# Kernel optimization log

Hardware: AMD Instinct MI355X
Metric: run time of the kernel (lower is better)

## Reference

```python
import jax, jax.numpy as jnp
import numpy as np

B, C, H, W = 1, 320, 64, 64
HEADS, DHEAD = 8, 40
INNER = HEADS * DHEAD          # 320 == C (as in Stable Diffusion)
CTX_LEN, CTX_DIM = 77, 768
FF_INNER = 4 * INNER           # 1280
GROUPS, GN_EPS, LN_EPS = 32, 1e-6, 1e-5
SCALE = DHEAD ** -0.5


def setup_inputs() -> dict:
    key = jax.random.key(0)
    ks = jax.random.split(key, 16)
    def w(k, shape):
        return jax.random.normal(k, shape, jnp.float32) * 0.02
    return {
        'x': jax.random.normal(ks[0], (B, C, H, W), jnp.float32),
        'context': jax.random.normal(ks[1], (B, CTX_LEN, CTX_DIM), jnp.float32),
        'gn_scale': jnp.ones((C,), jnp.float32),
        'gn_bias': jnp.zeros((C,), jnp.float32),
        'w_proj_in': w(ks[2], (C, INNER)), 'b_proj_in': jnp.zeros((INNER,), jnp.float32),
        'ln1_s': jnp.ones((INNER,), jnp.float32), 'ln1_b': jnp.zeros((INNER,), jnp.float32),
        'wq1': w(ks[3], (INNER, INNER)), 'wk1': w(ks[4], (INNER, INNER)),
        'wv1': w(ks[5], (INNER, INNER)), 'wo1': w(ks[6], (INNER, INNER)),
        'bo1': jnp.zeros((INNER,), jnp.float32),
        'ln2_s': jnp.ones((INNER,), jnp.float32), 'ln2_b': jnp.zeros((INNER,), jnp.float32),
        'wq2': w(ks[7], (INNER, INNER)), 'wk2': w(ks[8], (CTX_DIM, INNER)),
        'wv2': w(ks[9], (CTX_DIM, INNER)), 'wo2': w(ks[10], (INNER, INNER)),
        'bo2': jnp.zeros((INNER,), jnp.float32),
        'ln3_s': jnp.ones((INNER,), jnp.float32), 'ln3_b': jnp.zeros((INNER,), jnp.float32),
        'w_ff1': w(ks[11], (INNER, 2 * FF_INNER)), 'b_ff1': jnp.zeros((2 * FF_INNER,), jnp.float32),
        'w_ff2': w(ks[12], (FF_INNER, INNER)), 'b_ff2': jnp.zeros((INNER,), jnp.float32),
        'w_proj_out': w(ks[13], (INNER, C)), 'b_proj_out': jnp.zeros((C,), jnp.float32),
    }


def _group_norm(x, scale, bias):
    b, c, h, w = x.shape
    xg = x.reshape(b, GROUPS, c // GROUPS, h, w)
    mu = xg.mean(axis=(2, 3, 4), keepdims=True)
    var = xg.var(axis=(2, 3, 4), keepdims=True)
    xg = (xg - mu) * jax.lax.rsqrt(var + GN_EPS)
    return xg.reshape(b, c, h, w) * scale[None, :, None, None] + bias[None, :, None, None]


def _layer_norm(x, s, b):
    mu = x.mean(-1, keepdims=True)
    var = x.var(-1, keepdims=True)
    return (x - mu) * jax.lax.rsqrt(var + LN_EPS) * s + b


def _attention(xq, ctx, wq, wk, wv, wo, bo):
    b, s, _ = xq.shape
    t = ctx.shape[1]
    q = (xq @ wq).reshape(b, s, HEADS, DHEAD)
    k = (ctx @ wk).reshape(b, t, HEADS, DHEAD)
    v = (ctx @ wv).reshape(b, t, HEADS, DHEAD)
    scores = jnp.einsum('bihd,bjhd->bhij', q, k) * SCALE  # [b,h,s,t]
    probs = jax.nn.softmax(scores, axis=-1)
    o = jnp.einsum('bhij,bjhd->bihd', probs, v).reshape(b, s, INNER)
    return o @ wo + bo


def _forward(x, context, gn_scale, gn_bias, w_proj_in, b_proj_in,
             ln1_s, ln1_b, wq1, wk1, wv1, wo1, bo1,
             ln2_s, ln2_b, wq2, wk2, wv2, wo2, bo2,
             ln3_s, ln3_b, w_ff1, b_ff1, w_ff2, b_ff2,
             w_proj_out, b_proj_out):
    x_in = x
    h_ = _group_norm(x, gn_scale, gn_bias)
    # 1x1 conv proj_in as channel matmul
    h_ = jnp.einsum('bchw,cd->bdhw', h_, w_proj_in) + b_proj_in[None, :, None, None]
    h_ = h_.transpose(0, 2, 3, 1).reshape(B, H * W, INNER)  # [b, s, d]
    # self-attention
    hn = _layer_norm(h_, ln1_s, ln1_b)
    h_ = _attention(hn, hn, wq1, wk1, wv1, wo1, bo1) + h_
    # cross-attention
    hn = _layer_norm(h_, ln2_s, ln2_b)
    h_ = _attention(hn, context, wq2, wk2, wv2, wo2, bo2) + h_
    # GEGLU feed-forward
    hn = _layer_norm(h_, ln3_s, ln3_b)
    y = hn @ w_ff1 + b_ff1
    a, g = jnp.split(y, 2, axis=-1)
    y = (a * jax.nn.gelu(g, approximate=False)) @ w_ff2 + b_ff2
    h_ = y + h_
    h_ = h_.reshape(B, H, W, INNER).transpose(0, 3, 1, 2)
    out = jnp.einsum('bchw,cd->bdhw', h_, w_proj_out) + b_proj_out[None, :, None, None]
    return out + x_in


def reference(x, context, gn_scale, gn_bias, w_proj_in, b_proj_in,
              ln1_s, ln1_b, wq1, wk1, wv1, wo1, bo1,
              ln2_s, ln2_b, wq2, wk2, wv2, wo2, bo2,
              ln3_s, ln3_b, w_ff1, b_ff1, w_ff2, b_ff2,
              w_proj_out, b_proj_out):
    return _forward(x, context, gn_scale, gn_bias, w_proj_in, b_proj_in,
                    ln1_s, ln1_b, wq1, wk1, wv1, wo1, bo1,
                    ln2_s, ln2_b, wq2, wk2, wv2, wo2, bo2,
                    ln3_s, ln3_b, w_ff1, b_ff1, w_ff2, b_ff2,
                    w_proj_out, b_proj_out)
```

## Files before the change

### kernel.cpp

```cpp
#include <hip/hip_runtime.h>
#include <hip/hip_bf16.h>
#include <math.h>

#define SCALE_L2E  0.22811011265722836f

typedef __attribute__((ext_vector_type(8))) short short8v;
typedef __attribute__((ext_vector_type(4))) float float4v;
typedef unsigned short u16;

__device__ __forceinline__ unsigned pack2(float a, float b) {
  float2 f; f.x = a; f.y = b;
  __hip_bfloat162 h = __float22bfloat162_rn(f);
  return *(unsigned*)&h;
}
__device__ __forceinline__ float bfu2f(u16 u) {
  return __uint_as_float(((unsigned)u) << 16);
}
__device__ __forceinline__ u16 f2bf(float x) {
  __hip_bfloat16 h = __float2bfloat16(x);
  return *(u16*)&h;
}

struct TDesc { const float* src; u16* dst; int K, N, off, tx; float sc; };
struct TPack { TDesc d[12]; };

__global__ __launch_bounds__(256) void prep_kernel(
    TPack p, int nT,
    const float* __restrict__ ctxsrc, u16* __restrict__ ctxdst,
    const float* __restrict__ x,
    float* __restrict__ psum, float* __restrict__ psq) {
  __shared__ float ls[32][33];
  int bt = blockIdx.x, t = threadIdx.x;
  if (bt < nT) {
    int ti = 0;
    #pragma unroll
    for (int i = 1; i < 12; i++) if (bt >= p.d[i].off) ti = i;
    TDesc dd = p.d[ti];
    int local = bt - dd.off;
    int n0 = (local % dd.tx) * 32, k0 = (local / dd.tx) * 32;
    #pragma unroll
    for (int i = 0; i < 4; i++) {
      int idx = t + i*256, r = idx >> 5, c = idx & 31;
      ls[r][c] = dd.src[(size_t)(k0 + r)*dd.N + n0 + c];
    }
    __syncthreads();
    #pragma unroll
    for (int i = 0; i < 2; i++) {
      int p2 = t + i*256, n = p2 >> 4, kp = (p2 & 15)*2;
      *(unsigned*)&dd.dst[(size_t)(n0 + n)*dd.K + k0 + kp] =
        pack2(ls[kp][n]*dd.sc, ls[kp+1][n]*dd.sc);
    }
  } else if (bt < nT + 58) {
    int idx = ((bt - nT)*256 + t)*4;
    if (idx < 59136) {
      float4 v = *(const float4*)&ctxsrc[idx];
      uint2 o; o.x = pack2(v.x, v.y); o.y = pack2(v.z, v.w);
      *(uint2*)&ctxdst[idx] = o;
    }
  } else {
    int pp = bt - nT - 58;
    int g = pp >> 3, part = pp & 7;
    size_t base = (size_t)g*40960 + (size_t)part*5120;
    float sum = 0.f, sq = 0.f;
    #pragma unroll
    for (int r = 0; r < 5; r++) {
      float4 v = *(const float4*)&x[base + (size_t)(t + r*256)*4];
      sum += v.x + v.y + v.z + v.w;
      sq  += v.x*v.x + v.y*v.y + v.z*v.z + v.w*v.w;
    }
    float* s1 = &ls[0][0];
    float* s2 = &ls[8][0] + 8;
    s1[t] = sum; s2[t] = sq; __syncthreads();
    for (int st = 128; st > 0; st >>= 1) {
      if (t < st) { s1[t] += s1[t+st]; s2[t] += s2[t+st]; }
      __syncthreads();
    }
    if (t == 0) { psum[pp] = s1[0]; psq[pp] = s2[0]; }
  }
}

__global__ __launch_bounds__(256) void gn_kcvc(
    const float* __restrict__ x, const float* __restrict__ psum,
    const float* __restrict__ psq, const float* __restrict__ gs,
    const float* __restrict__ gb, u16* __restrict__ gnT,
    const u16* __restrict__ ctxb, const u16* __restrict__ wk2T,
    u16* __restrict__ kcvc) {
  __shared__ __align__(16) u16 smem[2*64*72];
  __shared__ float scl[64], sft[64];
  const int t = threadIdx.x;
  if (blockIdx.x < 320) {
    float* ts = (float*)smem;
    int s0 = (blockIdx.x & 63) * 64, c0 = (blockIdx.x >> 6) * 64;
    if (t < 64) {
      int c = c0 + t, g = c / 10;
      float s = 0.f, q = 0.f;
      #pragma unroll
      for (int i = 0; i < 8; i++) { s += psum[g*8 + i]; q += psq[g*8 + i]; }
      float mu = s * (1.f/40960.f);
      float var = q * (1.f/40960.f) - mu*mu;
      float rs = rsqrtf(var + 1e-6f);
      float sc = rs * gs[c];
      scl[t] = sc;
      sft[t] = gb[c] - mu * sc;
    }
    int crow = t >> 2, sch = (t & 3) * 16;
    #pragma unroll
    for (int j = 0; j < 4; j++) {
      float4 v = *(const float4*)&x[(size_t)(c0 + crow)*4096 + s0 + sch + 4*j];
      ts[crow*65 + sch + 4*j + 0] = v.x; ts[crow*65 + sch + 4*j + 1] = v.y;
      ts[crow*65 + sch + 4*j + 2] = v.z; ts[crow*65 + sch + 4*j + 3] = v.w;
    }
    __syncthreads();
    int srow = t >> 2, cch = (t & 3) * 16;
    #pragma unroll
    for (int p = 0; p < 8; p++) {
      int cl = cch + 2*p;
      float f0 = ts[cl*65 + srow] * scl[cl] + sft[cl];
      float f1 = ts[(cl+1)*65 + srow] * scl[cl+1] + sft[cl+1];
      *(unsigned*)&gnT[(size_t)(s0 + srow)*320 + c0 + cl] = pack2(f0, f1);
    }
  } else {
    u16* As = smem;
    u16* Bs = smem + 64*72;
    const int lane = t & 63, w = t >> 6, l16 = lane & 15, g = lane >> 4;
    int local = blockIdx.x - 320;
    const int bm = (local & 1) * 64, bn = (local >> 1) * 64;
    const int m0 = (w & 1) * 32, n0 = (w >> 1) * 32;
    float4v acc[2][2] = {};
    const int ar = t >> 2, ac = (t & 3) * 16;
    const bool aok = (bm + ar) < 77;
    const u16* ga = &ctxb[(size_t)(bm + ar)*768 + ac];
    const u16* gbp = &wk2T[(size_t)(bn + ar)*768 + ac];
    short8v pa0 = {}, pa1 = {}, pb0, pb1;
    if (aok) { pa0 = *(const short8v*)ga; pa1 = *(const short8v*)(ga + 8); }
    pb0 = *(const short8v*)gbp; pb1 = *(const short8v*)(gbp + 8);
    for (int k0 = 0; k0 < 768; k0 += 64) {
      __syncthreads();
      *(short8v*)&As[ar*72 + ac] = pa0;
      *(short8v*)&As[ar*72 + ac + 8] = pa1;
      *(short8v*)&Bs[ar*72 + ac] = pb0;
      *(short8v*)&Bs[ar*72 + ac + 8] = pb1;
      __syncthreads();
      if (k0 + 64 < 768) {
        if (aok) { pa0 = *(const short8v*)(ga + k0 + 64); pa1 = *(const short8v*)(ga + k0 + 72); }
        pb0 = *(const short8v*)(gbp + k0 + 64); pb1 = *(const short8v*)(gbp + k0 + 72);
      }
      #pragma unroll
      for (int ks = 0; ks < 2; ks++) {
        short8v af[2], bfv[2];
        #pragma unroll
        for (int mt = 0; mt < 2; mt++)
          af[mt] = *(const short8v*)&As[(m0 + 16*mt + l16)*72 + ks*32 + g*8];
        #pragma unroll
        for (int nt = 0; nt < 2; nt++)
          bfv[nt] = *(const short8v*)&Bs[(n0 + 16*nt + l16)*72 + ks*32 + g*8];
        #pragma unroll
        for (int mt = 0; mt < 2; mt++)
          #pragma unroll
          for (int nt = 0; nt < 2; nt++)
            acc[mt][nt] = __builtin_amdgcn_mfma_f32_16x16x32_bf16(af[mt], bfv[nt], acc[mt][nt], 0, 0, 0);
      }
    }
    __syncthreads();
    float* Cs = (float*)smem;
    #pragma unroll
    for (int mt = 0; mt < 2; mt++)
      #pragma unroll
      for (int nt = 0; nt < 2; nt++)
        #pragma unroll
        for (int r = 0; r < 4; r++)
          Cs[(m0 + 16*mt + 4*g + r)*68 + n0 + 16*nt + l16] = acc[mt][nt][r];
    __syncthreads();
    u16* C = kcvc + (size_t)(bn / 320) * 24640;
    int nb = bn % 320;
    #pragma unroll
    for (int i = 0; i < 8; i++) {
      int p = t + i*256;
      int mm = p >> 5, nn = (p & 31)*2;
      if (bm + mm >= 77) continue;
      *(unsigned*)&C[(size_t)(bm + mm)*320 + nb + nn] = pack2(Cs[mm*68 + nn], Cs[mm*68 + nn + 1]);
    }
  }
}

__global__ __launch_bounds__(64) void layernorm_kernel(
    const u16* __restrict__ X, const float* __restrict__ s,
    const float* __restrict__ b, u16* __restrict__ Y) {
  int row = blockIdx.x, t = threadIdx.x;
  const u16* xr = X + (size_t)row*320;
  float v[5], sum = 0.f, sq = 0.f;
  #pragma unroll
  for (int i = 0; i < 5; i++) { v[i] = bfu2f(xr[t + 64*i]); sum += v[i]; sq += v[i]*v[i]; }
  #pragma unroll
  for (int o = 32; o > 0; o >>= 1) { sum += __shfl_down(sum, o); sq += __shfl_down(sq, o); }
  sum = __shfl(sum, 0); sq = __shfl(sq, 0);
  float mu = sum * (1.f/320.f);
  float var = sq * (1.f/320.f) - mu*mu;
  float rs = rsqrtf(var + 1e-5f);
  u16* yr = Y + (size_t)row*320;
  #pragma unroll
  for (int i = 0; i < 5; i++) {
    int c = t + 64*i;
    yr[c] = f2bf((v[i]-mu)*rs*s[c] + b[c]);
  }
}

template<int MODE>
__global__ __launch_bounds__(256) void oneshot(
    const u16* __restrict__ A, const u16* __restrict__ BT,
    const float* __restrict__ bias, const u16* __restrict__ res,
    const float* __restrict__ xres, void* __restrict__ Cout,
    int K, int chunks) {
  __shared__ __align__(16) u16 As[64*328];
  __shared__ __align__(16) u16 Bs[32*328];
  const int t = threadIdx.x;
  const int lane = t & 63, w = t >> 6, l16 = lane & 15, g = lane >> 4;
  const int bm = blockIdx.x * 64, bn = blockIdx.y * 32;
  const int m0 = (w & 1) * 32, n0 = (w >> 1) * 16;
  float4v acc[2] = {};

  const u16* Ab = A + (size_t)(bm + (t>>2))*K + (t&3)*16;
  u16* Al = As + (t>>2)*328 + (t&3)*16;
  const u16* Bb = BT + (size_t)(bn + (t>>3))*K + (t&7)*16;
  u16* Bl = Bs + (t>>3)*328 + (t&7)*16;
  const bool b3 = (t & 7) < 4;

  for (int ch = 0; ch < chunks; ch++) {
    const int c0 = ch*320;
    __syncthreads();
    #pragma unroll
    for (int j = 0; j < 5; j++) {
      *(short8v*)(Al + 64*j)     = *(const short8v*)(Ab + c0 + 64*j);
      *(short8v*)(Al + 64*j + 8) = *(const short8v*)(Ab + c0 + 64*j + 8);
    }
    *(short8v*)Bl         = *(const short8v*)(Bb + c0);
    *(short8v*)(Bl + 8)   = *(const short8v*)(Bb + c0 + 8);
    *(short8v*)(Bl + 128) = *(const short8v*)(Bb + c0 + 128);
    *(short8v*)(Bl + 136) = *(const short8v*)(Bb + c0 + 136);
    if (b3) {
      *(short8v*)(Bl + 256) = *(const short8v*)(Bb + c0 + 256);
      *(short8v*)(Bl + 264) = *(const short8v*)(Bb + c0 + 264);
    }
    __syncthreads();
    #pragma unroll
    for (int ks = 0; ks < 10; ks++) {
      short8v bfv = *(const short8v*)&Bs[(n0 + l16)*328 + ks*32 + g*8];
      #pragma unroll
      for (int mt = 0; mt < 2; mt++) {
        short8v af = *(const short8v*)&As[(m0 + 16*mt + l16)*328 + ks*32 + g*8];
        acc[mt] = __builtin_amdgcn_mfma_f32_16x16x32_bf16(af, bfv, acc[mt], 0, 0, 0);
      }
    }
  }
  __syncthreads();
  float* Cs = (float*)As;
  #pragma unroll
  for (int mt = 0; mt < 2; mt++)
    #pragma unroll
    for (int r = 0; r < 4; r++)
      Cs[(m0 + 16*mt + 4*g + r)*36 + n0 + l16] = acc[mt][r];
  __syncthreads();

  if (MODE == 0) {
    u16* C = (u16*)Cout;
    #pragma unroll
    for (int i = 0; i < 4; i++) {
      int p = t + i*256;
      int mm = p >> 4, pp = (p & 15)*2;
      float f0 = Cs[mm*36 + pp], f1 = Cs[mm*36 + pp + 1];
      if (bias) { f0 += bias[bn + pp]; f1 += bias[bn + pp + 1]; }
      if (res) {
        unsigned u = *(const unsigned*)&res[(size_t)(bm + mm)*320 + bn + pp];
        f0 += bfu2f((u16)(u & 0xffffu));
        f1 += bfu2f((u16)(u >> 16));
      }
      *(unsigned*)&C[(size_t)(bm + mm)*320 + bn + pp] = pack2(f0, f1);
    }
  } else {
    float* C = (float*)Cout;
    int nloc = t >> 3, mch = (t & 7) * 8;
    float bb = bias[bn + nloc];
    #pragma unroll
    for (int j = 0; j < 2; j++) {
      int m4 = mch + j*4;
      float4 xv = *(const float4*)&xres[(size_t)(bn + nloc)*4096 + bm + m4];
      float4 ov;
      ov.x = Cs[(m4+0)*36 + nloc] + bb + xv.x;
      ov.y = Cs[(m4+1)*36 + nloc] + bb + xv.y;
      ov.z = Cs[(m4+2)*36 + nloc] + bb + xv.z;
      ov.w = Cs[(m4+3)*36 + nloc] + bb + xv.w;
      *(float4*)&C[(size_t)(bn + nloc)*4096 + bm + m4] = ov;
    }
  }
}

__global__ __launch_bounds__(256) void qkv_oneshot(
    const u16* __restrict__ A, const u16* __restrict__ BT,
    u16* __restrict__ qk, u16* __restrict__ vT, int segStride) {
  __shared__ __align__(16) u16 As[64*328];
  __shared__ __align__(16) u16 Bs[32*328];
  const int t = threadIdx.x;
  const int lane = t & 63, w = t >> 6, l16 = lane & 15, g = lane >> 4;
  const int bm = blockIdx.x * 64, bn = blockIdx.y * 32;
  const int m0 = (w & 1) * 32, n0 = (w >> 1) * 16;
  float4v acc[2] = {};

  const u16* Ab = A + (size_t)(bm + (t>>2))*320 + (t&3)*16;
  u16* Al = As + (t>>2)*328 + (t&3)*16;
  const u16* Bb = BT + (size_t)(bn + (t>>3))*320 + (t&7)*16;
  u16* Bl = Bs + (t>>3)*328 + (t&7)*16;
  const bool b3 = (t & 7) < 4;

  #pragma unroll
  for (int j = 0; j < 5; j++) {
    *(short8v*)(Al + 64*j)     = *(const short8v*)(Ab + 64*j);
    *(short8v*)(Al + 64*j + 8) = *(const short8v*)(Ab + 64*j + 8);
  }
  *(short8v*)Bl         = *(const short8v*)Bb;
  *(short8v*)(Bl + 8)   = *(const short8v*)(Bb + 8);
  *(short8v*)(Bl + 128) = *(const short8v*)(Bb + 128);
  *(short8v*)(Bl + 136) = *(const short8v*)(Bb + 136);
  if (b3) {
    *(short8v*)(Bl + 256) = *(const short8v*)(Bb + 256);
    *(short8v*)(Bl + 264) = *(const short8v*)(Bb + 264);
  }
  __syncthreads();
  #pragma unroll
  for (int ks = 0; ks < 10; ks++) {
    short8v bfv = *(const short8v*)&Bs[(n0 + l16)*328 + ks*32 + g*8];
    #pragma unroll
    for (int mt = 0; mt < 2; mt++) {
      short8v af = *(const short8v*)&As[(m0 + 16*mt + l16)*328 + ks*32 + g*8];
      acc[mt] = __builtin_amdgcn_mfma_f32_16x16x32_bf16(af, bfv, acc[mt], 0, 0, 0);
    }
  }
  __syncthreads();
  float* Cs = (float*)As;
  #pragma unroll
  for (int mt = 0; mt < 2; mt++)
    #pragma unroll
    for (int r = 0; r < 4; r++)
      Cs[(m0 + 16*mt + 4*g + r)*36 + n0 + l16] = acc[mt][r];
  __syncthreads();

  if (bn < 640) {
    u16* C = qk + (size_t)(bn / 320) * segStride;
    int nb = bn % 320;
    #pragma unroll
    for (int i = 0; i < 4; i++) {
      int p = t + i*256;
      int mm = p >> 4, pp = (p & 15)*2;
      *(unsigned*)&C[(size_t)(bm + mm)*320 + nb + pp] = pack2(Cs[mm*36 + pp], Cs[mm*36 + pp + 1]);
    }
  } else {
    int nloc = t >> 3, mch = (t & 7) * 8;
    int vd = bn - 640 + nloc;
    u16* dst = vT + (size_t)vd*4096 + bm + mch;
    uint4 o0;
    o0.x = pack2(Cs[(mch+0)*36 + nloc], Cs[(mch+1)*36 + nloc]);
    o0.y = pack2(Cs[(mch+2)*36 + nloc], Cs[(mch+3)*36 + nloc]);
    o0.z = pack2(Cs[(mch+4)*36 + nloc], Cs[(mch+5)*36 + nloc]);
    o0.w = pack2(Cs[(mch+6)*36 + nloc], Cs[(mch+7)*36 + nloc]);
    *(uint4*)dst = o0;
  }
}

__global__ __launch_bounds__(256) void geglu_mfma(
    const u16* __restrict__ A, const u16* __restrict__ BT,
    const float* __restrict__ bias, u16* __restrict__ C) {
  __shared__ __align__(16) u16 smem[3*64*72];
  u16* As = smem;
  u16* Ba = smem + 64*72;
  u16* Bg = smem + 2*64*72;
  const int t = threadIdx.x;
  const int lane = t & 63, w = t >> 6, l16 = lane & 15, g = lane >> 4;
  const int bm = blockIdx.x * 64, bn = blockIdx.y * 64;
  const int m0 = (w & 1) * 32, n0 = (w >> 1) * 32;
  float4v aacc[2][2] = {}, gacc[2][2] = {};
  const int ar = t >> 2, ac = (t & 3) * 16;
  const u16* ga  = &A[(size_t)(bm + ar)*320 + ac];
  const u16* gba = &BT[(size_t)(bn + ar)*320 + ac];
  const u16* gbg = &BT[(size_t)(1280 + bn + ar)*320 + ac];

  short8v pa0 = *(const short8v*)ga,  pa1 = *(const short8v*)(ga + 8);
  short8v pb0 = *(const short8v*)gba, pb1 = *(const short8v*)(gba + 8);
  short8v pg0 = *(const short8v*)gbg, pg1 = *(const short8v*)(gbg + 8);

  for (int k0 = 0; k0 < 320; k0 += 64) {
    __syncthreads();
    *(short8v*)&As[ar*72 + ac] = pa0;
    *(short8v*)&As[ar*72 + ac + 8] = pa1;
    *(short8v*)&Ba[ar*72 + ac] = pb0;
    *(short8v*)&Ba[ar*72 + ac + 8] = pb1;
    *(short8v*)&Bg[ar*72 + ac] = pg0;
    *(short8v*)&Bg[ar*72 + ac + 8] = pg1;
    __syncthreads();
    if (k0 + 64 < 320) {
      pa0 = *(const short8v*)(ga + k0 + 64);  pa1 = *(const short8v*)(ga + k0 + 72);
      pb0 = *(const short8v*)(gba + k0 + 64); pb1 = *(const short8v*)(gba + k0 + 72);
      pg0 = *(const short8v*)(gbg + k0 + 64); pg1 = *(const short8v*)(gbg + k0 + 72);
    }
    #pragma unroll
    for (int ks = 0; ks < 2; ks++) {
      short8v af[2], bav[2], bgv[2];
      #pragma unroll
      for (int mt = 0; mt < 2; mt++)
        af[mt] = *(const short8v*)&As[(m0 + 16*mt + l16)*72 + ks*32 + g*8];
      #pragma unroll
      for (int nt = 0; nt < 2; nt++) {
        bav[nt] = *(const short8v*)&Ba[(n0 + 16*nt + l16)*72 + ks*32 + g*8];
        bgv[nt] = *(const short8v*)&Bg[(n0 + 16*nt + l16)*72 + ks*32 + g*8];
      }
      #pragma unroll
      for (int mt = 0; mt < 2; mt++)
        #pragma unroll
        for (int nt = 0; nt < 2; nt++) {
          aacc[mt][nt] = __builtin_amdgcn_mfma_f32_16x16x32_bf16(af[mt], bav[nt], aacc[mt][nt], 0, 0, 0);
          gacc[mt][nt] = __builtin_amdgcn_mfma_f32_16x16x32_bf16(af[mt], bgv[nt], gacc[mt][nt], 0, 0, 0);
        }
    }
  }
  __syncthreads();
  float* Cs = (float*)smem;
  #pragma unroll
  for (int nt = 0; nt < 2; nt++) {
    int col = n0 + 16*nt + l16;
    float ba = bias[bn + col];
    float bg2 = bias[1280 + bn + col];
    #pragma unroll
    for (int mt = 0; mt < 2; mt++)
      #pragma unroll
      for (int r = 0; r < 4; r++) {
        float a = aacc[mt][nt][r] + ba;
        float gv = gacc[mt][nt][r] + bg2;
        float gl = 0.5f * gv * (1.f + erff(gv * 0.70710678118654752f));
        Cs[(m0 + 16*mt + 4*g + r)*68 + col] = a * gl;
      }
  }
  __syncthreads();
  #pragma unroll
  for (int i = 0; i < 8; i++) {
    int p = t + i*256;
    int mm = p >> 5, nn = (p & 31)*2;
    *(unsigned*)&C[(size_t)(bm + mm)*1280 + bn + nn] = pack2(Cs[mm*68 + nn], Cs[mm*68 + nn + 1]);
  }
}

__global__ __launch_bounds__(512) void self_attn_part(
    const u16* __restrict__ Q, const u16* __restrict__ K,
    const u16* __restrict__ vT, u16* __restrict__ Opart,
    float* __restrict__ Lp) {
  const int h = blockIdx.y;
  const int q0 = blockIdx.x * 128;
  const int sp = blockIdx.z;
  const int tid = threadIdx.x;
  const int w = tid >> 6, lane = tid & 63;
  const int l16 = lane & 15, g = lane >> 4;

  __shared__ __align__(16) u16 Kls[64][72];
  __shared__ __align__(16) u16 Vt[48][72];
  __shared__ __align__(16) u16 PsT[8][16][72];

  for (int e = tid; e < 64*12; e += 512) {
    int r = e / 12, c = e % 12;
    *(unsigned*)&Kls[r][40 + 2*c] = 0u;
  }
  if (tid < 256) {
    int r = 40 + (tid >> 5), c = tid & 31;
    *(unsigned*)&Vt[r][2*c] = (r == 40) ? 0x3F803F80u : 0u;
  }

  short8v Qb[2];
  {
    const u16* qrow = Q + (size_t)(q0 + w*16 + l16)*320 + h*40;
    Qb[0] = *(const short8v*)(qrow + g*8);
    short8v z = {};
    Qb[1] = (g == 0) ? *(const short8v*)(qrow + 32) : z;
  }

  const u16* Kbase = K + (size_t)(sp*1024)*320 + h*40;
  const u16* Vbase = vT + (size_t)(h*40)*4096 + sp*1024;

  const int ksl = (tid < 320) ? tid : 0;
  const int keyK = ksl / 5, chK = ksl - keyK*5;
  const u16* gK = Kbase + (size_t)keyK*320 + chK*8;
  u16* lK = &Kls[keyK][chK*8];
  const int vsl = (tid >= 192) ? (tid - 192) : 0;
  const int dV = vsl >> 3, chV = vsl & 7;
  const u16* gV = Vbase + (size_t)dV*4096 + chV*8;
  u16* lV = &Vt[dV][chV*8];

  const bool doK = (tid < 320), doV = (tid >= 192);

  short8v rK = {}, rV = {};
  if (doK) rK = *(const short8v*)gK;
  if (doV) rV = *(const short8v*)gV;
  gK += 64*320; gV += 64;

  float4v Of[3] = {};

  for (int it = 0; it < 16; ++it) {
    __syncthreads();
    if (doK) *(short8v*)lK = rK;
    if (doV) *(short8v*)lV = rV;
    __syncthreads();
    if (it < 15) {
      if (doK) rK = *(const short8v*)gK;
      if (doV) rV = *(const short8v*)gV;
      gK += 64*320; gV += 64;
    }

    float4v Sf[4];
    #pragma unroll
    for (int mt = 0; mt < 4; mt++) {
      short8v ka0 = *(const short8v*)&Kls[mt*16 + l16][g*8];
      short8v ka1 = *(const short8v*)&Kls[mt*16 + l16][32 + g*8];
      float4v s = {};
      s = __builtin_amdgcn_mfma_f32_16x16x32_bf16(ka0, Qb[0], s, 0, 0, 0);
      s = __builtin_amdgcn_mfma_f32_16x16x32_bf16(ka1, Qb[1], s, 0, 0, 0);
      Sf[mt] = s;
    }

    #pragma unroll
    for (int mt = 0; mt < 4; mt++)
      #pragma unroll
      for (int r = 0; r < 4; r++)
        Sf[mt][r] = exp2f(Sf[mt][r]);

    #pragma unroll
    for (int mt = 0; mt < 4; mt++) {
      uint2 pk;
      pk.x = pack2(Sf[mt][0], Sf[mt][1]);
      pk.y = pack2(Sf[mt][2], Sf[mt][3]);
      *(uint2*)&PsT[w][l16][mt*16 + 4*g] = pk;
    }
    asm volatile("s_waitcnt lgkmcnt(0)" ::: "memory");

    #pragma unroll
    for (int ks = 0; ks < 2; ks++) {
      short8v pb = *(const short8v*)&PsT[w][l16][ks*32 + g*8];
      #pragma unroll
      for (int mt = 0; mt < 3; mt++) {
        short8v va = *(const short8v*)&Vt[mt*16 + l16][ks*32 + g*8];
        Of[mt] = __builtin_amdgcn_mfma_f32_16x16x32_bf16(va, pb, Of[mt], 0, 0, 0);
      }
    }
  }

  const int q = q0 + w*16 + l16;
  u16* orow = Opart + (size_t)sp*4096*320 + (size_t)q*320 + h*40;
  #pragma unroll
  for (int mt = 0; mt < 3; mt++) {
    #pragma unroll
    for (int rp = 0; rp < 2; rp++) {
      int d = mt*16 + 4*g + rp*2;
      if (d < 40)
        *(unsigned*)&orow[d] = pack2(Of[mt][rp*2], Of[mt][rp*2+1]);
    }
  }
  if (g == 2)
    Lp[sp*32768 + q*8 + h] = Of[2][0];
}

__global__ __launch_bounds__(256) void attn_merge(
    const u16* __restrict__ Opart, const float* __restrict__ Lp,
    u16* __restrict__ O) {
  int gid = blockIdx.x*256 + threadIdx.x;
  int dp = gid % 20;
  int qh = gid / 20;
  int q = qh >> 3, h = qh & 7;
  float ls = Lp[qh] + Lp[32768 + qh] + Lp[2*32768 + qh] + Lp[3*32768 + qh];
  size_t base = (size_t)q*320 + h*40 + dp*2;
  const size_t HBu = 4096u*320u;
  float r0 = 0.f, r1 = 0.f;
  #pragma unroll
  for (int sp = 0; sp < 4; sp++) {
    unsigned u = *(const unsigned*)&Opart[sp*HBu + base];
    r0 += bfu2f((u16)(u & 0xffffu));
    r1 += bfu2f((u16)(u >> 16));
  }
  float inv = 1.f / ls;
  *(unsigned*)&O[base] = pack2(r0*inv, r1*inv);
}

__global__ __launch_bounds__(256) void cross_attn_mfma(
    const u16* __restrict__ Q, const u16* __restrict__ Kc,
    const u16* __restrict__ Vc, u16* __restrict__ O) {
  const int h = blockIdx.y;
  const int q0 = blockIdx.x * 64;
  const int tid = threadIdx.x;
  const int w = tid >> 6, lane = tid & 63;
  const int l16 = lane & 15, g = lane >> 4;

  __shared__ __align__(16) u16 Kls[80][72];
  __shared__ __align__(16) u16 Vt[48][104];
  __shared__ __align__(16) u16 PsT[4][16][104];

  for (int e = tid; e < 80*12; e += 256) {
    int r = e / 12, c = e % 12;
    *(unsigned*)&Kls[r][40 + 2*c] = 0u;
  }
  for (int e = tid; e < 48*52; e += 256) {
    int r = e / 52, c = e % 52;
    *(unsigned*)&Vt[r][2*c] = 0u;
  }
  {
    int r = lane >> 2, c4 = (lane & 3)*4;
    uint2 z; z.x = 0u; z.y = 0u;
    *(uint2*)&PsT[w][r][80 + c4] = z;
  }

  short8v Qb[2];
  {
    const u16* qrow = Q + (size_t)(q0 + w*16 + l16)*320 + h*40;
    Qb[0] = *(const short8v*)(qrow + g*8);
    short8v z = {};
    Qb[1] = (g == 0) ? *(const short8v*)(qrow + 32) : z;
  }

  for (int e = tid; e < 1600; e += 256) {
    int key = e / 20, dp = e % 20;
    unsigned val = 0u;
    if (key < 77) val = *(const unsigned*)&Kc[(size_t)key*320 + h*40 + dp*2];
    *(unsigned*)&Kls[key][dp*2] = val;
  }
  __syncthreads();
  for (int e = tid; e < 1600; e += 256) {
    int kp = e / 40, d = e % 40;
    unsigned u0 = (kp*2     < 77) ? (unsigned)Vc[(size_t)(kp*2    )*320 + h*40 + d] : 0u;
    unsigned u1 = (kp*2 + 1 < 77) ? (unsigned)Vc[(size_t)(kp*2 + 1)*320 + h*40 + d] : 0u;
    *(unsigned*)&Vt[d][kp*2] = u0 | (u1 << 16);
  }
  __syncthreads();

  float4v Sf[5];
  #pragma unroll
  for (int mt = 0; mt < 5; mt++) {
    short8v ka0 = *(const short8v*)&Kls[mt*16 + l16][g*8];
    short8v ka1 = *(const short8v*)&Kls[mt*16 + l16][32 + g*8];
    float4v s = {};
    s = __builtin_amdgcn_mfma_f32_16x16x32_bf16(ka0, Qb[0], s, 0, 0, 0);
    s = __builtin_amdgcn_mfma_f32_16x16x32_bf16(ka1, Qb[1], s, 0, 0, 0);
    Sf[mt] = s;
  }

  float rsum = 0.f;
  #pragma unroll
  for (int mt = 0; mt < 5; mt++)
    #pragma unroll
    for (int r = 0; r < 4; r++) {
      int key = mt*16 + 4*g + r;
      float p = (key < 77) ? exp2f(Sf[mt][r]) : 0.f;
      Sf[mt][r] = p; rsum += p;
    }
  rsum += __shfl_xor(rsum, 16);
  rsum += __shfl_xor(rsum, 32);

  #pragma unroll
  for (int mt = 0; mt < 5; mt++) {
    uint2 pk;
    pk.x = pack2(Sf[mt][0], Sf[mt][1]);
    pk.y = pack2(Sf[mt][2], Sf[mt][3]);
    *(uint2*)&PsT[w][l16][mt*16 + 4*g] = pk;
  }
  __syncthreads();

  float4v Of[3] = {};
  #pragma unroll
  for (int ks = 0; ks < 3; ks++) {
    short8v pb = *(const short8v*)&PsT[w][l16][ks*32 + g*8];
    #pragma unroll
    for (int mt = 0; mt < 3; mt++) {
      short8v va = *(const short8v*)&Vt[mt*16 + l16][ks*32 + g*8];
      Of[mt] = __builtin_amdgcn_mfma_f32_16x16x32_bf16(va, pb, Of[mt], 0, 0, 0);
    }
  }

  float inv = 1.f / rsum;
  u16* orow = O + (size_t)(q0 + w*16 + l16)*320 + h*40;
  #pragma unroll
  for (int mt = 0; mt < 3; mt++) {
    #pragma unroll
    for (int rp = 0; rp < 2; rp++) {
      int d = mt*16 + 4*g + rp*2;
      if (d < 40)
        *(unsigned*)&orow[d] = pack2(Of[mt][rp*2] * inv, Of[mt][rp*2+1] * inv);
    }
  }
}

extern "C" void kernel_launch(void* const* d_in, const int* in_sizes, int n_in,
                              void* d_out, int out_size, void* d_ws, size_t ws_size,
                              hipStream_t stream) {
  const float* x        = (const float*)d_in[0];
  const float* ctx      = (const float*)d_in[1];
  const float* gn_s     = (const float*)d_in[2];
  const float* gn_b     = (const float*)d_in[3];
  const float* w_pin    = (const float*)d_in[4];
  const float* b_pin    = (const float*)d_in[5];
  const float* ln1_s    = (const float*)d_in[6];
  const float* ln1_b    = (const float*)d_in[7];
  const float* wq1      = (const float*)d_in[8];
  const float* wk1      = (const float*)d_in[9];
  const float* wv1      = (const float*)d_in[10];
  const float* wo1      = (const float*)d_in[11];
  const float* bo1      = (const float*)d_in[12];
  const float* ln2_s    = (const float*)d_in[13];
  const float* ln2_b    = (const float*)d_in[14];
  const float* wq2      = (const float*)d_in[15];
  const float* wk2      = (const float*)d_in[16];
  const float* wv2      = (const float*)d_in[17];
  const float* wo2      = (const float*)d_in[18];
  const float* bo2      = (const float*)d_in[19];
  const float* ln3_s    = (const float*)d_in[20];
  const float* ln3_b    = (const float*)d_in[21];
  const float* w_ff1    = (const float*)d_in[22];
  const float* b_ff1    = (const float*)d_in[23];
  const float* w_ff2    = (const float*)d_in[24];
  const float* b_ff2    = (const float*)d_in[25];
  const float* w_pout   = (const float*)d_in[26];
  const float* b_pout   = (const float*)d_in[27];
  float* out = (float*)d_out;

  u16* ws = (u16*)d_ws;
  const size_t HB = 4096u*320u;
  u16* h   = ws;
  u16* hn  = ws + HB;
  u16* q   = ws + 2*HB;
  u16* k   = ws + 3*HB;
  u16* vT  = ws + 4*HB;
  u16* ao  = ws + 5*HB;
  u16* gnT = k;
  u16* gg  = q;
  u16* wb  = ws + 6*HB;
  size_t o = 0;
  u16* ctxb   = wb + o; o += 59136;
  u16* wq1T   = wb + o; o += 102400;
  u16* wk1T   = wb + o; o += 102400;
  u16* wv1T   = wb + o; o += 102400;
  u16* wo1T   = wb + o; o += 102400;
  u16* wq2T   = wb + o; o += 102400;
  u16* wk2T   = wb + o; o += 245760;
  u16* wv2T   = wb + o; o += 245760;
  u16* wo2T   = wb + o; o += 102400;
  u16* wff1T  = wb + o; o += 819200;
  u16* wff2T  = wb + o; o += 409600;
  u16* wpoutT = wb + o; o += 102400;
  u16* wpinT  = wb + o; o += 102400;
  u16* kc     = wb + o; o += 24640;
  u16* vc     = wb + o; o += 24640;
  float* psum = (float*)(wb + o);
  float* psq  = psum + 256;
  u16* OpartB = (u16*)(psq + 256);
  float* Lpart = (float*)(OpartB + 4*HB);

  TPack tp;
  const float* srcs[12] = {wq1, wk1, wv1, wo1, wq2, wo2, w_pin, w_pout, wk2, wv2, w_ff1, w_ff2};
  u16* dsts[12]         = {wq1T, wk1T, wv1T, wo1T, wq2T, wo2T, wpinT, wpoutT, wk2T, wv2T, wff1T, wff2T};
  int Ks[12] = {320,320,320,320,320,320,320,320,768,768,320,1280};
  int Ns[12] = {320,320,320,320,320,320,320,320,320,320,2560,320};
  int off = 0;
  for (int i = 0; i < 12; i++) {
    tp.d[i].src = srcs[i]; tp.d[i].dst = dsts[i];
    tp.d[i].K = Ks[i]; tp.d[i].N = Ns[i];
    tp.d[i].off = off; tp.d[i].tx = Ns[i]/32;
    tp.d[i].sc = (i == 0 || i == 4) ? SCALE_L2E : 1.0f;
    off += (Ks[i]/32)*(Ns[i]/32);
  }

  dim3 blk(256), g64x10(64, 10);
  const u16* nres = nullptr;
  const float* nb = nullptr;

  hipLaunchKernelGGL(prep_kernel, dim3(off + 58 + 256), blk, 0, stream,
                     tp, off, ctx, ctxb, x, psum, psq);
  hipLaunchKernelGGL(gn_kcvc, dim3(340), blk, 0, stream,
                     x, psum, psq, gn_s, gn_b, gnT, ctxb, wk2T, kc);
  hipLaunchKernelGGL((oneshot<0>), g64x10, blk, 0, stream, gnT, wpinT, b_pin, nres, nb, (void*)h, 320, 1);
  hipLaunchKernelGGL(layernorm_kernel, dim3(4096), dim3(64), 0, stream, h, ln1_s, ln1_b, hn);
  hipLaunchKernelGGL(qkv_oneshot, dim3(64, 30), blk, 0, stream, hn, wq1T, q, vT, (int)HB);
  hipLaunchKernelGGL(self_attn_part, dim3(32, 8, 4), dim3(512), 0, stream, q, k, vT, OpartB, Lpart);
  hipLaunchKernelGGL(attn_merge, dim3(2560), blk, 0, stream, OpartB, Lpart, ao);
  hipLaunchKernelGGL((oneshot<0>), g64x10, blk, 0, stream, ao, wo1T, bo1, h, nb, (void*)h, 320, 1);
  hipLaunchKernelGGL(layernorm_kernel, dim3(4096), dim3(64), 0, stream, h, ln2_s, ln2_b, hn);
  hipLaunchKernelGGL((oneshot<0>), g64x10, blk, 0, stream, hn, wq2T, nb, nres, nb, (void*)q, 320, 1);
  hipLaunchKernelGGL(cross_attn_mfma, dim3(64, 8), blk, 0, stream, q, kc, vc, ao);
  hipLaunchKernelGGL((oneshot<0>), g64x10, blk, 0, stream, ao, wo2T, bo2, h, nb, (void*)h, 320, 1);
  hipLaunchKernelGGL(layernorm_kernel, dim3(4096), dim3(64), 0, stream, h, ln3_s, ln3_b, hn);
  hipLaunchKernelGGL(geglu_mfma, dim3(64, 20), blk, 0, stream, hn, wff1T, b_ff1, gg);
  hipLaunchKernelGGL((oneshot<0>), g64x10, blk, 0, stream, gg, wff2T, b_ff2, h, nb, (void*)h, 1280, 4);
  hipLaunchKernelGGL((oneshot<2>), g64x10, blk, 0, stream, h, wpoutT, b_pout, nres, x, (void*)out, 320, 1);
}
```

Measured before the change: 289.7 us.

## Fuse LayerNorm into consuming GEMMs by folding affine params into weights

Removes the three standalone LayerNorm kernels and their bf16 round-trip through the hn buffer. The LN gain is folded into the transposed weight columns during prep, and the LN bias is folded into a per-output bias vector (W^T·b) computed by extra prep blocks. The consuming GEMMs (qkv, q2, geglu) now normalise each loaded row in registers before staging it to LDS. This trades extra per-block normalisation work (each output-column tile recomputes the row statistics) and a slightly different rounding order for fewer launches and less global memory traffic.

Measured after the change: 298.5 us. 3.0% more time.

```diff
diff --git a/kernel.cpp b/kernel.cpp
--- a/kernel.cpp
+++ b/kernel.cpp
@@ -16,16 +16,44 @@
 __device__ __forceinline__ float bfu2f(u16 u) {
   return __uint_as_float(((unsigned)u) << 16);
 }
-__device__ __forceinline__ u16 f2bf(float x) {
-  __hip_bfloat16 h = __float2bfloat16(x);
-  return *(u16*)&h;
-}
-
-struct TDesc { const float* src; u16* dst; int K, N, off, tx; float sc; };
+
+__device__ __forceinline__ void row_ln(short8v av[10]) {
+  float sum = 0.f, sq = 0.f;
+  #pragma unroll
+  for (int v = 0; v < 10; v++) {
+    union { short8v s; u16 u[8]; } t; t.s = av[v];
+    #pragma unroll
+    for (int e = 0; e < 8; e++) {
+      float f = bfu2f(t.u[e]);
+      sum += f; sq = fmaf(f, f, sq);
+    }
+  }
+  sum += __shfl_xor(sum, 1); sum += __shfl_xor(sum, 2);
+  sq  += __shfl_xor(sq, 1);  sq  += __shfl_xor(sq, 2);
+  float mu = sum * (1.f/320.f);
+  float var = sq * (1.f/320.f) - mu*mu;
+  float rs = rsqrtf(var + 1e-5f);
+  float cc = -mu * rs;
+  #pragma unroll
+  for (int v = 0; v < 10; v++) {
+    union { short8v s; u16 u[8]; unsigned w[4]; } t; t.s = av[v];
+    #pragma unroll
+    for (int e = 0; e < 4; e++) {
+      float f0 = fmaf(bfu2f(t.u[2*e]),   rs, cc);
+      float f1 = fmaf(bfu2f(t.u[2*e+1]), rs, cc);
+      t.w[e] = pack2(f0, f1);
+    }
+    av[v] = t.s;
+  }
+}
+
+struct TDesc { const float* src; u16* dst; const float* sv; int K, N, off, tx; float sc; };
 struct TPack { TDesc d[12]; };
+struct GDesc { const float* W; const float* bvec; const float* add; float* out; int K, N, off; float sc; };
+struct GPack { GDesc d[5]; };
 
 __global__ __launch_bounds__(256) void prep_kernel(
-    TPack p, int nT,
+    TPack p, GPack gp, int nT,
     const float* __restrict__ ctxsrc, u16* __restrict__ ctxdst,
     const float* __restrict__ x,
     float* __restrict__ psum, float* __restrict__ psq) {
@@ -47,8 +75,10 @@
     #pragma unroll
     for (int i = 0; i < 2; i++) {
       int p2 = t + i*256, n = p2 >> 4, kp = (p2 & 15)*2;
+      float s0 = dd.sc, s1 = dd.sc;
+      if (dd.sv) { s0 *= dd.sv[k0 + kp]; s1 *= dd.sv[k0 + kp + 1]; }
       *(unsigned*)&dd.dst[(size_t)(n0 + n)*dd.K + k0 + kp] =
-        pack2(ls[kp][n]*dd.sc, ls[kp+1][n]*dd.sc);
+        pack2(ls[kp][n]*s0, ls[kp+1][n]*s1);
     }
   } else if (bt < nT + 58) {
     int idx = ((bt - nT)*256 + t)*4;
@@ -57,7 +87,7 @@
       uint2 o; o.x = pack2(v.x, v.y); o.y = pack2(v.z, v.w);
       *(uint2*)&ctxdst[idx] = o;
     }
-  } else {
+  } else if (bt < nT + 58 + 256) {
     int pp = bt - nT - 58;
     int g = pp >> 3, part = pp & 7;
     size_t base = (size_t)g*40960 + (size_t)part*5120;
@@ -76,6 +106,22 @@
       __syncthreads();
     }
     if (t == 0) { psum[pp] = s1[0]; psq[pp] = s2[0]; }
+  } else {
+    int bg = bt - nT - 58 - 256;
+    int gi = 0;
+    #pragma unroll
+    for (int i = 1; i < 5; i++) if (bg >= gp.d[i].off) gi = i;
+    GDesc dd = gp.d[gi];
+    int n = (bg - dd.off)*256 + t;
+    if (n < dd.N) {
+      float acc = 0.f;
+      #pragma unroll 8
+      for (int k = 0; k < dd.K; k++)
+        acc = fmaf(dd.W[(size_t)k*dd.N + n], dd.bvec[k], acc);
+      acc *= dd.sc;
+      if (dd.add) acc += dd.add[n];
+      dd.out[n] = acc;
+    }
   }
 }
 
@@ -183,29 +229,7 @@
   }
 }
 
-__global__ __launch_bounds__(64) void layernorm_kernel(
-    const u16* __restrict__ X, const float* __restrict__ s,
-    const float* __restrict__ b, u16* __restrict__ Y) {
-  int row = blockIdx.x, t = threadIdx.x;
-  const u16* xr = X + (size_t)row*320;
-  float v[5], sum = 0.f, sq = 0.f;
-  #pragma unroll
-  for (int i = 0; i < 5; i++) { v[i] = bfu2f(xr[t + 64*i]); sum += v[i]; sq += v[i]*v[i]; }
-  #pragma unroll
-  for (int o = 32; o > 0; o >>= 1) { sum += __shfl_down(sum, o); sq += __shfl_down(sq, o); }
-  sum = __shfl(sum, 0); sq = __shfl(sq, 0);
-  float mu = sum * (1.f/320.f);
-  float var = sq * (1.f/320.f) - mu*mu;
-  float rs = rsqrtf(var + 1e-5f);
-  u16* yr = Y + (size_t)row*320;
-  #pragma unroll
-  for (int i = 0; i < 5; i++) {
-    int c = t + 64*i;
-    yr[c] = f2bf((v[i]-mu)*rs*s[c] + b[c]);
-  }
-}
-
-template<int MODE>
+template<int MODE, int LN>
 __global__ __launch_bounds__(256) void oneshot(
     const u16* __restrict__ A, const u16* __restrict__ BT,
     const float* __restrict__ bias, const u16* __restrict__ res,
@@ -228,10 +252,25 @@
   for (int ch = 0; ch < chunks; ch++) {
     const int c0 = ch*320;
     __syncthreads();
-    #pragma unroll
-    for (int j = 0; j < 5; j++) {
-      *(short8v*)(Al + 64*j)     = *(const short8v*)(Ab + c0 + 64*j);
-      *(short8v*)(Al + 64*j + 8) = *(const short8v*)(Ab + c0 + 64*j + 8);
+    if (LN) {
+      short8v av[10];
+      #pragma unroll
+      for (int j = 0; j < 5; j++) {
+        av[2*j]   = *(const short8v*)(Ab + 64*j);
+        av[2*j+1] = *(const short8v*)(Ab + 64*j + 8);
+      }
+      row_ln(av);
+      #pragma unroll
+      for (int j = 0; j < 5; j++) {
+        *(short8v*)(Al + 64*j)     = av[2*j];
+        *(short8v*)(Al + 64*j + 8) = av[2*j+1];
+      }
+    } else {
+      #pragma unroll
+      for (int j = 0; j < 5; j++) {
+        *(short8v*)(Al + 64*j)     = *(const short8v*)(Ab + c0 + 64*j);
+        *(short8v*)(Al + 64*j + 8) = *(const short8v*)(Ab + c0 + 64*j + 8);
+      }
     }
     *(short8v*)Bl         = *(const short8v*)(Bb + c0);
     *(short8v*)(Bl + 8)   = *(const short8v*)(Bb + c0 + 8);
@@ -296,7 +335,8 @@
 
 __global__ __launch_bounds__(256) void qkv_oneshot(
     const u16* __restrict__ A, const u16* __restrict__ BT,
-    u16* __restrict__ qk, u16* __restrict__ vT, int segStride) {
+    const float* __restrict__ fb, u16* __restrict__ qk, u16* __restrict__ vT,
+    int segStride) {
   __shared__ __align__(16) u16 As[64*328];
   __shared__ __align__(16) u16 Bs[32*328];
   const int t = threadIdx.x;
@@ -311,10 +351,19 @@
   u16* Bl = Bs + (t>>3)*328 + (t&7)*16;
   const bool b3 = (t & 7) < 4;
 
-  #pragma unroll
-  for (int j = 0; j < 5; j++) {
-    *(short8v*)(Al + 64*j)     = *(const short8v*)(Ab + 64*j);
-    *(short8v*)(Al + 64*j + 8) = *(const short8v*)(Ab + 64*j + 8);
+  {
+    short8v av[10];
+    #pragma unroll
+    for (int j = 0; j < 5; j++) {
+      av[2*j]   = *(const short8v*)(Ab + 64*j);
+      av[2*j+1] = *(const short8v*)(Ab + 64*j + 8);
+    }
+    row_ln(av);
+    #pragma unroll
+    for (int j = 0; j < 5; j++) {
+      *(short8v*)(Al + 64*j)     = av[2*j];
+      *(short8v*)(Al + 64*j + 8) = av[2*j+1];
+    }
   }
   *(short8v*)Bl         = *(const short8v*)Bb;
   *(short8v*)(Bl + 8)   = *(const short8v*)(Bb + 8);
@@ -350,17 +399,20 @@
     for (int i = 0; i < 4; i++) {
       int p = t + i*256;
       int mm = p >> 4, pp = (p & 15)*2;
-      *(unsigned*)&C[(size_t)(bm + mm)*320 + nb + pp] = pack2(Cs[mm*36 + pp], Cs[mm*36 + pp + 1]);
+      float f0 = Cs[mm*36 + pp] + fb[bn + pp];
+      float f1 = Cs[mm*36 + pp + 1] + fb[bn + pp + 1];
+      *(unsigned*)&C[(size_t)(bm + mm)*320 + nb + pp] = pack2(f0, f1);
     }
   } else {
     int nloc = t >> 3, mch = (t & 7) * 8;
     int vd = bn - 640 + nloc;
+    float bb = fb[bn + nloc];
     u16* dst = vT + (size_t)vd*4096 + bm + mch;
     uint4 o0;
-    o0.x = pack2(Cs[(mch+0)*36 + nloc], Cs[(mch+1)*36 + nloc]);
-    o0.y = pack2(Cs[(mch+2)*36 + nloc], Cs[(mch+3)*36 + nloc]);
-    o0.z = pack2(Cs[(mch+4)*36 + nloc], Cs[(mch+5)*36 + nloc]);
-    o0.w = pack2(Cs[(mch+6)*36 + nloc], Cs[(mch+7)*36 + nloc]);
+    o0.x = pack2(Cs[(mch+0)*36 + nloc] + bb, Cs[(mch+1)*36 + nloc] + bb);
+    o0.y = pack2(Cs[(mch+2)*36 + nloc] + bb, Cs[(mch+3)*36 + nloc] + bb);
+    o0.z = pack2(Cs[(mch+4)*36 + nloc] + bb, Cs[(mch+5)*36 + nloc] + bb);
+    o0.w = pack2(Cs[(mch+6)*36 + nloc] + bb, Cs[(mch+7)*36 + nloc] + bb);
     *(uint4*)dst = o0;
   }
 }
@@ -382,21 +434,27 @@
   const u16* gba = &BT[(size_t)(bn + ar)*320 + ac];
   const u16* gbg = &BT[(size_t)(1280 + bn + ar)*320 + ac];
 
-  short8v pa0 = *(const short8v*)ga,  pa1 = *(const short8v*)(ga + 8);
+  short8v av[10];
+  #pragma unroll
+  for (int j = 0; j < 5; j++) {
+    av[2*j]   = *(const short8v*)(ga + 64*j);
+    av[2*j+1] = *(const short8v*)(ga + 64*j + 8);
+  }
+  row_ln(av);
+
   short8v pb0 = *(const short8v*)gba, pb1 = *(const short8v*)(gba + 8);
   short8v pg0 = *(const short8v*)gbg, pg1 = *(const short8v*)(gbg + 8);
 
   for (int k0 = 0; k0 < 320; k0 += 64) {
     __syncthreads();
-    *(short8v*)&As[ar*72 + ac] = pa0;
-    *(short8v*)&As[ar*72 + ac + 8] = pa1;
+    *(short8v*)&As[ar*72 + ac] = av[2*(k0>>6)];
+    *(short8v*)&As[ar*72 + ac + 8] = av[2*(k0>>6)+1];
     *(short8v*)&Ba[ar*72 + ac] = pb0;
     *(short8v*)&Ba[ar*72 + ac + 8] = pb1;
     *(short8v*)&Bg[ar*72 + ac] = pg0;
     *(short8v*)&Bg[ar*72 + ac + 8] = pg1;
     __syncthreads();
     if (k0 + 64 < 320) {
-      pa0 = *(const short8v*)(ga + k0 + 64);  pa1 = *(const short8v*)(ga + k0 + 72);
       pb0 = *(const short8v*)(gba + k0 + 64); pb1 = *(const short8v*)(gba + k0 + 72);
       pg0 = *(const short8v*)(gbg + k0 + 64); pg1 = *(const short8v*)(gbg + k0 + 72);
     }
@@ -725,7 +783,6 @@
   u16* ws = (u16*)d_ws;
   const size_t HB = 4096u*320u;
   u16* h   = ws;
-  u16* hn  = ws + HB;
   u16* q   = ws + 2*HB;
   u16* k   = ws + 3*HB;
   u16* vT  = ws + 4*HB;
@@ -751,43 +808,60 @@
   u16* vc     = wb + o; o += 24640;
   float* psum = (float*)(wb + o);
   float* psq  = psum + 256;
-  u16* OpartB = (u16*)(psq + 256);
+  float* fbqkv = psq + 256;
+  float* fbq2  = fbqkv + 960;
+  float* fbffc = fbq2 + 320;
+  u16* OpartB = (u16*)(fbffc + 2560);
   float* Lpart = (float*)(OpartB + 4*HB);
 
   TPack tp;
   const float* srcs[12] = {wq1, wk1, wv1, wo1, wq2, wo2, w_pin, w_pout, wk2, wv2, w_ff1, w_ff2};
   u16* dsts[12]         = {wq1T, wk1T, wv1T, wo1T, wq2T, wo2T, wpinT, wpoutT, wk2T, wv2T, wff1T, wff2T};
+  const float* svs[12]  = {ln1_s, ln1_s, ln1_s, nullptr, ln2_s, nullptr, nullptr, nullptr,
+                           nullptr, nullptr, ln3_s, nullptr};
   int Ks[12] = {320,320,320,320,320,320,320,320,768,768,320,1280};
   int Ns[12] = {320,320,320,320,320,320,320,320,320,320,2560,320};
   int off = 0;
   for (int i = 0; i < 12; i++) {
-    tp.d[i].src = srcs[i]; tp.d[i].dst = dsts[i];
+    tp.d[i].src = srcs[i]; tp.d[i].dst = dsts[i]; tp.d[i].sv = svs[i];
     tp.d[i].K = Ks[i]; tp.d[i].N = Ns[i];
     tp.d[i].off = off; tp.d[i].tx = Ns[i]/32;
     tp.d[i].sc = (i == 0 || i == 4) ? SCALE_L2E : 1.0f;
     off += (Ks[i]/32)*(Ns[i]/32);
   }
 
+  GPack gp;
+  const float* gW[5]  = {wq1, wk1, wv1, wq2, w_ff1};
+  const float* gB[5]  = {ln1_b, ln1_b, ln1_b, ln2_b, ln3_b};
+  const float* gA[5]  = {nullptr, nullptr, nullptr, nullptr, b_ff1};
+  float* gO[5]        = {fbqkv, fbqkv + 320, fbqkv + 640, fbq2, fbffc};
+  int gN[5]           = {320, 320, 320, 320, 2560};
+  float gS[5]         = {SCALE_L2E, 1.f, 1.f, SCALE_L2E, 1.f};
+  int goff = 0;
+  for (int i = 0; i < 5; i++) {
+    gp.d[i].W = gW[i]; gp.d[i].bvec = gB[i]; gp.d[i].add = gA[i];
+    gp.d[i].out = gO[i]; gp.d[i].K = 320; gp.d[i].N = gN[i];
+    gp.d[i].off = goff; gp.d[i].sc = gS[i];
+    goff += (gN[i] + 255) / 256;
+  }
+
   dim3 blk(256), g64x10(64, 10);
   const u16* nres = nullptr;
   const float* nb = nullptr;
 
-  hipLaunchKernelGGL(prep_kernel, dim3(off + 58 + 256), blk, 0, stream,
-                     tp, off, ctx, ctxb, x, psum, psq);
+  hipLaunchKernelGGL(prep_kernel, dim3(off + 58 + 256 + goff), blk, 0, stream,
+                     tp, gp, off, ctx, ctxb, x, psum, psq);
   hipLaunchKernelGGL(gn_kcvc, dim3(340), blk, 0, stream,
                      x, psum, psq, gn_s, gn_b, gnT, ctxb, wk2T, kc);
-  hipLaunchKernelGGL((oneshot<0>), g64x10, blk, 0, stream, gnT, wpinT, b_pin, nres, nb, (void*)h, 320, 1);
-  hipLaunchKernelGGL(layernorm_kernel, dim3(4096), dim3(64), 0, stream, h, ln1_s, ln1_b, hn);
-  hipLaunchKernelGGL(qkv_oneshot, dim3(64, 30), blk, 0, stream, hn, wq1T, q, vT, (int)HB);
+  hipLaunchKernelGGL((oneshot<0,0>), g64x10, blk, 0, stream, gnT, wpinT, b_pin, nres, nb, (void*)h, 320, 1);
+  hipLaunchKernelGGL(qkv_oneshot, dim3(64, 30), blk, 0, stream, h, wq1T, fbqkv, q, vT, (int)HB);
   hipLaunchKernelGGL(self_attn_part, dim3(32, 8, 4), dim3(512), 0, stream, q, k, vT, OpartB, Lpart);
   hipLaunchKernelGGL(attn_merge, dim3(2560), blk, 0, stream, OpartB, Lpart, ao);
-  hipLaunchKernelGGL((oneshot<0>), g64x10, blk, 0, stream, ao, wo1T, bo1, h, nb, (void*)h, 320, 1);
-  hipLaunchKernelGGL(layernorm_kernel, dim3(4096), dim3(64), 0, stream, h, ln2_s, ln2_b, hn);
-  hipLaunchKernelGGL((oneshot<0>), g64x10, blk, 0, stream, hn, wq2T, nb, nres, nb, (void*)q, 320, 1);
+  hipLaunchKernelGGL((oneshot<0,0>), g64x10, blk, 0, stream, ao, wo1T, bo1, h, nb, (void*)h, 320, 1);
+  hipLaunchKernelGGL((oneshot<0,1>), g64x10, blk, 0, stream, h, wq2T, fbq2, nres, nb, (void*)q, 320, 1);
   hipLaunchKernelGGL(cross_attn_mfma, dim3(64, 8), blk, 0, stream, q, kc, vc, ao);
-  hipLaunchKernelGGL((oneshot<0>), g64x10, blk, 0, stream, ao, wo2T, bo2, h, nb, (void*)h, 320, 1);
-  hipLaunchKernelGGL(layernorm_kernel, dim3(4096), dim3(64), 0, stream, h, ln3_s, ln3_b, hn);
-  hipLaunchKernelGGL(geglu_mfma, dim3(64, 20), blk, 0, stream, hn, wff1T, b_ff1, gg);
-  hipLaunchKernelGGL((oneshot<0>), g64x10, blk, 0, stream, gg, wff2T, b_ff2, h, nb, (void*)h, 1280, 4);
-  hipLaunchKernelGGL((oneshot<2>), g64x10, blk, 0, stream, h, wpoutT, b_pout, nres, x, (void*)out, 320, 1);
-}
+  hipLaunchKernelGGL((oneshot<0,0>), g64x10, blk, 0, stream, ao, wo2T, bo2, h, nb, (void*)h, 320, 1);
+  hipLaunchKernelGGL(geglu_mfma, dim3(64, 20), blk, 0, stream, h, wff1T, fbffc, gg);
+  hipLaunchKernelGGL((oneshot<0,0>), g64x10, blk, 0, stream, gg, wff2T, b_ff2, h, nb, (void*)h, 1280, 4);
+  hipLaunchKernelGGL((oneshot<2,0>), g64x10, blk, 0, stream, h, wpoutT, b_pout, nres, x, (void*)out, 320, 1);
+}
```
